# Kernel tuning notes

Measured on AMD Instinct MI355X. Metric: run time of the kernel, lower is better.

Reference implementation:

```python
import jax, jax.numpy as jnp
import numpy as np

B, CIN, H, W = 4, 128, 64, 64
PL, ATT, R = 256, 64, 16   # planes, planes//4, MD_R
STEPS = 6                   # TRAIN_STEPS default
EPS = 1e-6


def _l2norm(v, axis):
    return v / jnp.maximum(jnp.linalg.norm(v, axis=axis, keepdims=True), 1e-12)


def setup_inputs() -> dict:
    key = jax.random.key(0)
    ks = jax.random.split(key, 11)
    s = 0.05
    return {
        "x": jax.random.normal(ks[0], (B, CIN, H, W), jnp.float32),
        "conv1_w": jax.random.normal(ks[1], (PL, CIN), jnp.float32) * s,      # 1x1 conv, no bias
        "conv3_w": jax.random.normal(ks[2], (PL, 1, 3, 3), jnp.float32) * s,  # depthwise 3x3
        "conv3_b": jax.random.normal(ks[3], (PL,), jnp.float32) * s,
        "lower_w": jax.random.normal(ks[4], (PL, PL), jnp.float32) * s,       # Conv1d k=1
        "lower_b": jax.random.normal(ks[5], (PL,), jnp.float32) * s,
        "ca1_w": jax.random.normal(ks[6], (ATT, PL), jnp.float32) * s,        # channel attn 1x1
        "ca2_w": jax.random.normal(ks[7], (PL, ATT), jnp.float32) * s,
        "fc_w": jax.random.normal(ks[8], (CIN, PL), jnp.float32) * s,         # fc_adapt_channels1
        "fc_b": jax.random.normal(ks[9], (CIN,), jnp.float32) * s,
        "bases_init": jax.random.uniform(ks[10], (B * H * W, 1, R), jnp.float32),  # rand_init bases
    }


def reference(x, conv1_w, conv3_w, conv3_b, lower_w, lower_b, ca1_w, ca2_w, fc_w, fc_b, bases_init):
    # conv1 (1x1, no bias) then depthwise 3x3 (groups=PL)
    y = jnp.einsum('bchw,oc->bohw', x, conv1_w)
    y = jax.lax.conv_general_dilated(y, conv3_w, (1, 1), 'SAME',
                                     dimension_numbers=('NCHW', 'OIHW', 'NCHW'),
                                     feature_group_count=PL)
    y = y + conv3_b[None, :, None, None]
    # '(b s) c h w -> (b h w) c s' with s=1 -> tokens [M, C]
    xm = jnp.transpose(y, (0, 2, 3, 1)).reshape(B * H * W, PL)
    # Hamburger lower_bread: Conv1d(k=1) + ReLU
    xl = jax.nn.relu(xm @ lower_w.T + lower_b)
    xn = xl[:, None, :]                        # NMF x: [M, D=1, N=C]
    # NMF2D local_inference (torch.no_grad in original)
    xs = jax.lax.stop_gradient(xn)
    bases = _l2norm(bases_init, 1)             # [M, 1, R]
    coef = jax.nn.softmax(jnp.einsum('mdn,mdr->mnr', xs, bases), axis=-1)  # inv_t=1
    for _ in range(STEPS):
        num = jnp.einsum('mdn,mdr->mnr', xs, bases)
        den = jnp.einsum('mnr,mrk->mnk', coef, jnp.einsum('mdr,mdk->mrk', bases, bases))
        coef = coef * num / (den + EPS)
        num = jnp.einsum('mdn,mnr->mdr', xs, coef)
        den = jnp.einsum('mdr,mrk->mdk', bases, jnp.einsum('mnr,mnk->mrk', coef, coef))
        bases = bases * num / (den + EPS)
    bases = jax.lax.stop_gradient(bases)
    coef = jax.lax.stop_gradient(coef)
    # compute_coef (differentiable via xn)
    num = jnp.einsum('mdn,mdr->mnr', xn, bases)
    den = jnp.einsum('mnr,mrk->mnk', coef, jnp.einsum('mdr,mdk->mrk', bases, bases))
    coef = coef * num / (den + EPS)
    xr = jnp.einsum('mdr,mnr->mn', bases, coef)     # bases @ coef^T, [M, C] (D=1 squeezed)
    feat = jax.nn.relu(xm + xr)                     # Hamburger residual + ReLU
    # mean over s (s=1) and back to [B, C, H, W]
    feat = jnp.transpose(feat.reshape(B, H, W, PL), (0, 3, 1, 2))
    # AMPooling channel attention
    avg = feat.mean(axis=(2, 3))
    mx = feat.max(axis=(2, 3))
    ca = lambda v: jax.nn.relu(v @ ca1_w.T) @ ca2_w.T
    att = jax.nn.sigmoid(ca(avg) + ca(mx))          # [B, C]
    out = feat * att[:, :, None, None]
    out = jnp.einsum('bchw,oc->bohw', out, fc_w) + fc_b[None, :, None, None]
    return out, att[:, :, None, None]
```

## Files before the change

### kernel.cpp

```cpp
#include <hip/hip_runtime.h>
#include <hip/hip_bf16.h>
#include <math.h>

#define EPS 1e-6f
#define PITCH 72

typedef short s16x8 __attribute__((ext_vector_type(8)));
typedef float f32x4 __attribute__((ext_vector_type(4)));

__device__ __forceinline__ short bf16of(float f) {
  __hip_bfloat16 h = __float2bfloat16(f);
  return __builtin_bit_cast(short, h);
}
__device__ __forceinline__ float f32of(unsigned short u) {
  unsigned int x = ((unsigned int)u) << 16;
  return __builtin_bit_cast(float, x);
}

__global__ __launch_bounds__(256) void k_conv1x1(const float* __restrict__ x,
                                                 const float* __restrict__ w1,
                                                 short* __restrict__ ybf) {
  __shared__ __align__(16) short Aw[128 * PITCH];
  __shared__ __align__(16) short Xs[64 * PITCH];
  const int t = threadIdx.x;
  const int m0 = blockIdx.x * 64, p0 = blockIdx.y * 128;
  const int img = m0 >> 12, hw0 = m0 & 4095;
  const int lane = t & 63, w = t >> 6;
  const int lrow = lane & 15, lk = (lane >> 4) * 8;
  f32x4 acc[4][2];
#pragma unroll
  for (int i = 0; i < 4; ++i)
#pragma unroll
    for (int j = 0; j < 2; ++j) acc[i][j] = {0.f, 0.f, 0.f, 0.f};

  for (int kk = 0; kk < 128; kk += 64) {
    __syncthreads();
    {
      const int pr = t & 127, kq = t >> 7;
      const float* wp = w1 + (size_t)(p0 + pr) * 128 + kk + kq * 32;
#pragma unroll
      for (int q = 0; q < 8; ++q) {
        const float4 v = *(const float4*)(wp + q * 4);
        short4 sv = {bf16of(v.x), bf16of(v.y), bf16of(v.z), bf16of(v.w)};
        *(short4*)(&Aw[pr * PITCH + kq * 32 + q * 4]) = sv;
      }
    }
    {
      const int m4 = (t & 15) * 4;
      const int cg = (t >> 4) * 4;
      float4 col[4];
#pragma unroll
      for (int cc = 0; cc < 4; ++cc)
        col[cc] = *(const float4*)(x + (size_t)(img * 128 + kk + cg + cc) * 4096 + hw0 + m4);
#pragma unroll
      for (int r = 0; r < 4; ++r) {
        short4 sv = {bf16of(((const float*)&col[0])[r]),
                     bf16of(((const float*)&col[1])[r]),
                     bf16of(((const float*)&col[2])[r]),
                     bf16of(((const float*)&col[3])[r])};
        *(short4*)(&Xs[(m4 + r) * PITCH + cg]) = sv;
      }
    }
    __syncthreads();
#pragma unroll
    for (int ks = 0; ks < 2; ++ks) {
      const int ko = ks * 32 + lk;
      s16x8 bfr[2];
#pragma unroll
      for (int j = 0; j < 2; ++j)
        bfr[j] = *(const s16x8*)(&Xs[(((w >> 1) * 2 + j) * 16 + lrow) * PITCH + ko]);
#pragma unroll
      for (int i = 0; i < 4; ++i) {
        const s16x8 af = *(const s16x8*)(&Aw[(((w & 1) * 4 + i) * 16 + lrow) * PITCH + ko]);
#pragma unroll
        for (int j = 0; j < 2; ++j)
          acc[i][j] = __builtin_amdgcn_mfma_f32_16x16x32_bf16(af, bfr[j], acc[i][j], 0, 0, 0);
      }
    }
  }
#pragma unroll
  for (int i = 0; i < 4; ++i) {
    const int p = p0 + ((w & 1) * 4 + i) * 16 + (lane >> 4) * 4;
#pragma unroll
    for (int j = 0; j < 2; ++j) {
      const int m = m0 + ((w >> 1) * 2 + j) * 16 + lrow;
      const f32x4 v = acc[i][j];
      short4 sv = {bf16of(v.x), bf16of(v.y), bf16of(v.z), bf16of(v.w)};
      *(short4*)(ybf + (size_t)m * 256 + p) = sv;
    }
  }
}

__global__ __launch_bounds__(256) void k_dwconv(const unsigned short* __restrict__ ybf,
                                                const float* __restrict__ w3,
                                                const float* __restrict__ b3,
                                                short* __restrict__ xmb) {
  __shared__ float wt[9][256];
  __shared__ float bs[256];
  const int t = threadIdx.x;
#pragma unroll
  for (int i = 0; i < 9; ++i) wt[i][t] = w3[t * 9 + i];
  bs[t] = b3[t];
  __syncthreads();
  const int sub = t >> 6;
  const int pq = t & 63;
  const int m = blockIdx.x * 4 + sub;
  const int hw = m & 4095;
  const int h = hw >> 6, ww = hw & 63;
  const int bb = m >> 12;
  float4 acc = *(const float4*)(&bs[pq * 4]);
#pragma unroll
  for (int dy = -1; dy <= 1; ++dy) {
    const int hh = h + dy;
    if (hh < 0 || hh > 63) continue;
#pragma unroll
    for (int dx = -1; dx <= 1; ++dx) {
      const int w2 = ww + dx;
      if (w2 < 0 || w2 > 63) continue;
      const int idx = (dy + 1) * 3 + (dx + 1);
      const ushort4 v =
          *(const ushort4*)(ybf + (size_t)((bb << 12) + (hh << 6) + w2) * 256 + pq * 4);
      const float4 wv = *(const float4*)(&wt[idx][pq * 4]);
      acc.x += f32of(v.x) * wv.x;
      acc.y += f32of(v.y) * wv.y;
      acc.z += f32of(v.z) * wv.z;
      acc.w += f32of(v.w) * wv.w;
    }
  }
  short4 sv = {bf16of(acc.x), bf16of(acc.y), bf16of(acc.z), bf16of(acc.w)};
  *(short4*)(xmb + (size_t)m * 256 + pq * 4) = sv;
}

__global__ __launch_bounds__(256) void k_lower(const unsigned short* __restrict__ xmb,
                                               const float* __restrict__ lw,
                                               const float* __restrict__ lb,
                                               short* __restrict__ xlb) {
  __shared__ __align__(16) short Aw[128 * PITCH];
  __shared__ __align__(16) short Xs[64 * PITCH];
  const int t = threadIdx.x;
  const int m0 = blockIdx.x * 64, n0 = blockIdx.y * 128;
  const int lane = t & 63, w = t >> 6;
  const int lrow = lane & 15, lk = (lane >> 4) * 8;
  f32x4 acc[4][2];
#pragma unroll
  for (int i = 0; i < 4; ++i)
#pragma unroll
    for (int j = 0; j < 2; ++j) acc[i][j] = {0.f, 0.f, 0.f, 0.f};

  for (int kk = 0; kk < 256; kk += 64) {
    __syncthreads();
    {
      const int nr = t & 127, kq = t >> 7;
      const float* wp = lw + (size_t)(n0 + nr) * 256 + kk + kq * 32;
#pragma unroll
      for (int q = 0; q < 8; ++q) {
        const float4 v = *(const float4*)(wp + q * 4);
        short4 sv = {bf16of(v.x), bf16of(v.y), bf16of(v.z), bf16of(v.w)};
        *(short4*)(&Aw[nr * PITCH + kq * 32 + q * 4]) = sv;
      }
    }
    {
      const int m = t & 63, q = t >> 6;
      const unsigned short* xp = xmb + (size_t)(m0 + m) * 256 + kk + q * 16;
      *(s16x8*)(&Xs[m * PITCH + q * 16]) = *(const s16x8*)(xp);
      *(s16x8*)(&Xs[m * PITCH + q * 16 + 8]) = *(const s16x8*)(xp + 8);
    }
    __syncthreads();
#pragma unroll
    for (int ks = 0; ks < 2; ++ks) {
      const int ko = ks * 32 + lk;
      s16x8 bfr[2];
#pragma unroll
      for (int j = 0; j < 2; ++j)
        bfr[j] = *(const s16x8*)(&Xs[(((w >> 1) * 2 + j) * 16 + lrow) * PITCH + ko]);
#pragma unroll
      for (int i = 0; i < 4; ++i) {
        const s16x8 af = *(const s16x8*)(&Aw[(((w & 1) * 4 + i) * 16 + lrow) * PITCH + ko]);
#pragma unroll
        for (int j = 0; j < 2; ++j)
          acc[i][j] = __builtin_amdgcn_mfma_f32_16x16x32_bf16(af, bfr[j], acc[i][j], 0, 0, 0);
      }
    }
  }
#pragma unroll
  for (int i = 0; i < 4; ++i) {
    const int n = n0 + ((w & 1) * 4 + i) * 16 + (lane >> 4) * 4;
    const float4 bias = *(const float4*)(lb + n);
#pragma unroll
    for (int j = 0; j < 2; ++j) {
      const int m = m0 + ((w >> 1) * 2 + j) * 16 + lrow;
      const f32x4 v = acc[i][j];
      short4 sv = {bf16of(fmaxf(v.x + bias.x, 0.f)), bf16of(fmaxf(v.y + bias.y, 0.f)),
                   bf16of(fmaxf(v.z + bias.z, 0.f)), bf16of(fmaxf(v.w + bias.w, 0.f))};
      *(short4*)(xlb + (size_t)m * 256 + n) = sv;
    }
  }
}

__global__ __launch_bounds__(256) void k_em_fast(const unsigned short* __restrict__ xlb,
                                                 const float* __restrict__ binit,
                                                 const unsigned short* __restrict__ xmb,
                                                 short* __restrict__ featb,
                                                 float* __restrict__ psum,
                                                 float* __restrict__ pmax,
                                                 int* __restrict__ flag) {
  __shared__ float psL[1024], pmL[1024];
  __shared__ int sflag;
  const int t = threadIdx.x;
  const int lane = t & 63, w = t >> 6;
  const int bid = blockIdx.x;
  const int m0 = bid * 16 + w * 4;
  bool asym = false;
#pragma unroll
  for (int p = 0; p < 4; ++p) {
    const float bv = binit[(size_t)(m0 + p) * 16 + (lane & 15)];
    const float bn = bv / fmaxf(fabsf(bv), 1e-12f);
    asym |= !__all(bn == 1.0f);
  }
  if (t == 0) sflag = 0;
  __syncthreads();
  if (asym && lane == 0) sflag = 1;
  __syncthreads();
  if (sflag) {
    if (t == 0) flag[bid] = 1;
    return;
  }

  float s[4][4], C[4][4], Bv[4];
#pragma unroll
  for (int p = 0; p < 4; ++p) {
    const ushort4 su = *(const ushort4*)(xlb + (size_t)(m0 + p) * 256 + lane * 4);
    s[p][0] = f32of(su.x);
    s[p][1] = f32of(su.y);
    s[p][2] = f32of(su.z);
    s[p][3] = f32of(su.w);
    Bv[p] = 1.f;
#pragma unroll
    for (int i = 0; i < 4; ++i) C[p][i] = 0.0625f;
  }
  for (int step = 0; step < 6; ++step) {
    float pnum[4], psq[4];
#pragma unroll
    for (int p = 0; p < 4; ++p) {
      const float k1 = 16.f * Bv[p] * Bv[p];
      pnum[p] = 0.f;
      psq[p] = 0.f;
#pragma unroll
      for (int i = 0; i < 4; ++i) {
        const float den = fmaf(C[p][i], k1, EPS);
        const float cn = C[p][i] * (s[p][i] * Bv[p]) * __builtin_amdgcn_rcpf(den);
        C[p][i] = cn;
        pnum[p] = fmaf(s[p][i], cn, pnum[p]);
        psq[p] = fmaf(cn, cn, psq[p]);
      }
    }
#pragma unroll
    for (int d = 1; d < 64; d <<= 1) {
#pragma unroll
      for (int p = 0; p < 4; ++p) {
        pnum[p] += __shfl_xor(pnum[p], d, 64);
        psq[p] += __shfl_xor(psq[p], d, 64);
      }
    }
#pragma unroll
    for (int p = 0; p < 4; ++p)
      Bv[p] = Bv[p] * pnum[p] *
              __builtin_amdgcn_rcpf(fmaf(16.f * Bv[p], psq[p], EPS));
  }
  float ps4[4] = {0.f, 0.f, 0.f, 0.f};
  float pm4[4] = {-1e30f, -1e30f, -1e30f, -1e30f};
#pragma unroll
  for (int p = 0; p < 4; ++p) {
    const ushort4 xmu = *(const ushort4*)(xmb + (size_t)(m0 + p) * 256 + lane * 4);
    const float xmv[4] = {f32of(xmu.x), f32of(xmu.y), f32of(xmu.z), f32of(xmu.w)};
    const float k1 = 16.f * Bv[p] * Bv[p];
    float o[4];
#pragma unroll
    for (int i = 0; i < 4; ++i) {
      const float den = fmaf(C[p][i], k1, EPS);
      const float cn = C[p][i] * (s[p][i] * Bv[p]) * __builtin_amdgcn_rcpf(den);
      const float xr = 16.f * Bv[p] * cn;
      o[i] = fmaxf(xmv[i] + xr, 0.f);
      ps4[i] += o[i];
      pm4[i] = fmaxf(pm4[i], o[i]);
    }
    short4 sv = {bf16of(o[0]), bf16of(o[1]), bf16of(o[2]), bf16of(o[3])};
    *(short4*)(featb + (size_t)(m0 + p) * 256 + lane * 4) = sv;
  }
#pragma unroll
  for (int i = 0; i < 4; ++i) {
    psL[w * 256 + lane * 4 + i] = ps4[i];
    pmL[w * 256 + lane * 4 + i] = pm4[i];
  }
  __syncthreads();
  const float sv = psL[t] + psL[256 + t] + psL[512 + t] + psL[768 + t];
  const float mv =
      fmaxf(fmaxf(pmL[t], pmL[256 + t]), fmaxf(pmL[512 + t], pmL[768 + t]));
  psum[(size_t)bid * 256 + t] = sv;
  pmax[(size_t)bid * 256 + t] = mv;
  if (t == 0) flag[bid] = 0;
}

__global__ __launch_bounds__(256, 2) void k_em_slowfix(
    const unsigned short* __restrict__ xlb, const float* __restrict__ binit,
    const unsigned short* __restrict__ xmb, short* __restrict__ featb,
    float* __restrict__ psum, float* __restrict__ pmax,
    const int* __restrict__ flag) {
  const int bid = blockIdx.x;
  if (flag[bid] == 0) return;
  __shared__ float psL[1024], pmL[1024];
  const int t = threadIdx.x;
  const int lane = t & 63, w = t >> 6;
  const int m0 = bid * 16 + w * 4;
  float ps4[4] = {0.f, 0.f, 0.f, 0.f};
  float pm4[4] = {-1e30f, -1e30f, -1e30f, -1e30f};
  for (int p = 0; p < 4; ++p) {
    const int m = m0 + p;
    const ushort4 su = *(const ushort4*)(xlb + (size_t)m * 256 + lane * 4);
    const float s[4] = {f32of(su.x), f32of(su.y), f32of(su.z), f32of(su.w)};
    float b[16];
#pragma unroll
    for (int r = 0; r < 16; ++r) {
      const float v = binit[(size_t)m * 16 + r];
      b[r] = v / fmaxf(fabsf(v), 1e-12f);
    }
    float c[4][16];
#pragma unroll
    for (int i = 0; i < 4; ++i) {
      float mx = s[i] * b[0];
#pragma unroll
      for (int r = 1; r < 16; ++r) mx = fmaxf(mx, s[i] * b[r]);
      float sum = 0.f;
#pragma unroll
      for (int r = 0; r < 16; ++r) {
        const float e = __expf(s[i] * b[r] - mx);
        c[i][r] = e;
        sum += e;
      }
      const float inv = __fdividef(1.f, sum);
#pragma unroll
      for (int r = 0; r < 16; ++r) c[i][r] *= inv;
    }
    for (int step = 0; step < 6; ++step) {
      float red[32];
#pragma unroll
      for (int r = 0; r < 32; ++r) red[r] = 0.f;
#pragma unroll
      for (int i = 0; i < 4; ++i) {
        float tt = 0.f;
#pragma unroll
        for (int r = 0; r < 16; ++r) tt += c[i][r] * b[r];
        float tp = 0.f;
#pragma unroll
        for (int r = 0; r < 16; ++r) {
          const float cn = c[i][r] * (s[i] * b[r]) * __frcp_rn(tt * b[r] + EPS);
          c[i][r] = cn;
          tp += cn * b[r];
          red[r] += s[i] * cn;
        }
#pragma unroll
        for (int r = 0; r < 16; ++r) red[16 + r] += tp * c[i][r];
      }
      int cnt = 32;
#pragma unroll
      for (int k = 4; k >= 0; --k) {
        const int d = 1 << k;
        const bool up = (lane >> k) & 1;
        const int half = cnt >> 1;
#pragma unroll
        for (int j = 0; j < half; ++j) {
          const float lo = red[j], hi = red[j + half];
          const float send = up ? lo : hi;
          const float recv = __shfl_xor(send, d, 64);
          red[j] = (up ? hi : lo) + recv;
        }
        cnt = half;
      }
      float S = red[0] + __shfl_xor(red[0], 32, 64);
      const float dpart = __shfl_xor(S, 16, 64);
      const float q = S * __frcp_rn(dpart + EPS);
#pragma unroll
      for (int r = 0; r < 16; ++r) b[r] *= __shfl(q, r, 64);
    }
    const ushort4 xmu = *(const ushort4*)(xmb + (size_t)m * 256 + lane * 4);
    const float xmv[4] = {f32of(xmu.x), f32of(xmu.y), f32of(xmu.z), f32of(xmu.w)};
    float o4[4];
#pragma unroll
    for (int i = 0; i < 4; ++i) {
      float tt = 0.f;
#pragma unroll
      for (int r = 0; r < 16; ++r) tt += c[i][r] * b[r];
      float xr = 0.f;
#pragma unroll
      for (int r = 0; r < 16; ++r) {
        const float cn = c[i][r] * (s[i] * b[r]) * __frcp_rn(tt * b[r] + EPS);
        xr += b[r] * cn;
      }
      o4[i] = fmaxf(xmv[i] + xr, 0.f);
      ps4[i] += o4[i];
      pm4[i] = fmaxf(pm4[i], o4[i]);
    }
    short4 sv = {bf16of(o4[0]), bf16of(o4[1]), bf16of(o4[2]), bf16of(o4[3])};
    *(short4*)(featb + (size_t)m * 256 + lane * 4) = sv;
  }
#pragma unroll
  for (int i = 0; i < 4; ++i) {
    psL[w * 256 + lane * 4 + i] = ps4[i];
    pmL[w * 256 + lane * 4 + i] = pm4[i];
  }
  __syncthreads();
  const float sv = psL[t] + psL[256 + t] + psL[512 + t] + psL[768 + t];
  const float mv =
      fmaxf(fmaxf(pmL[t], pmL[256 + t]), fmaxf(pmL[512 + t], pmL[768 + t]));
  psum[(size_t)bid * 256 + t] = sv;
  pmax[(size_t)bid * 256 + t] = mv;
}

__global__ __launch_bounds__(1024) void k_att(const float* __restrict__ psum,
                                              const float* __restrict__ pmax,
                                              const float* __restrict__ ca1,
                                              const float* __restrict__ ca2,
                                              float* __restrict__ attv,
                                              float* __restrict__ out_att) {
  __shared__ float sA[4][256], sM[4][256], fA[256], fM[256], sH[64];
  const int t = threadIdx.x;
  const int b = blockIdx.x;
  const int ch = t & 255, part = t >> 8;
  float sum = 0.f, mx = -1e30f;
#pragma unroll 4
  for (int j = 0; j < 64; ++j) {
    const int g = b * 256 + part * 64 + j;
    sum += psum[(size_t)g * 256 + ch];
    mx = fmaxf(mx, pmax[(size_t)g * 256 + ch]);
  }
  sA[part][ch] = sum;
  sM[part][ch] = mx;
  __syncthreads();
  if (t < 256) {
    fA[t] = (sA[0][t] + sA[1][t] + sA[2][t] + sA[3][t]) * (1.0f / 4096.0f);
    fM[t] = fmaxf(fmaxf(sM[0][t], sM[1][t]), fmaxf(sM[2][t], sM[3][t]));
  }
  __syncthreads();
  if (t < 64) {
    float ha = 0.f, hm = 0.f;
#pragma unroll 8
    for (int p = 0; p < 256; ++p) {
      const float wv = ca1[t * 256 + p];
      ha += fA[p] * wv;
      hm += fM[p] * wv;
    }
    sH[t] = fmaxf(ha, 0.f) + fmaxf(hm, 0.f);
  }
  __syncthreads();
  if (t < 256) {
    float logit = 0.f;
#pragma unroll 8
    for (int a = 0; a < 64; ++a) logit += sH[a] * ca2[t * 64 + a];
    const float av = 1.0f / (1.0f + expf(-logit));
    attv[b * 256 + t] = av;
    out_att[b * 256 + t] = av;
  }
}

__global__ __launch_bounds__(256) void k_fc(const unsigned short* __restrict__ featb,
                                            const float* __restrict__ attv,
                                            const float* __restrict__ fw,
                                            const float* __restrict__ fb,
                                            float* __restrict__ out) {
  __shared__ __align__(16) short Fs[64 * PITCH];
  __shared__ __align__(16) short Ws[64 * PITCH];
  const int t = threadIdx.x;
  const int m0 = blockIdx.x * 64, o0 = blockIdx.y * 64;
  const int img = m0 >> 12, hw0 = m0 & 4095;
  const int lane = t & 63, w = t >> 6;
  const int lrow = lane & 15, lk = (lane >> 4) * 8;
  f32x4 acc[2][2];
#pragma unroll
  for (int i = 0; i < 2; ++i)
#pragma unroll
    for (int j = 0; j < 2; ++j) acc[i][j] = {0.f, 0.f, 0.f, 0.f};

  for (int kk = 0; kk < 256; kk += 64) {
    __syncthreads();
    {
      const int m = t & 63, q = t >> 6;
      const unsigned short* fp = featb + (size_t)(m0 + m) * 256 + kk + q * 16;
      const float* ap = attv + img * 256 + kk + q * 16;
#pragma unroll
      for (int jj = 0; jj < 4; ++jj) {
        const ushort4 v = *(const ushort4*)(fp + jj * 4);
        const float4 a = *(const float4*)(ap + jj * 4);
        short4 sv = {bf16of(f32of(v.x) * a.x), bf16of(f32of(v.y) * a.y),
                     bf16of(f32of(v.z) * a.z), bf16of(f32of(v.w) * a.w)};
        *(short4*)(&Fs[m * PITCH + q * 16 + jj * 4]) = sv;
      }
    }
    {
      const int o = t & 63, q = t >> 6;
      const float* wp = fw + (size_t)(o0 + o) * 256 + kk + q * 16;
#pragma unroll
      for (int jj = 0; jj < 4; ++jj) {
        const float4 v = *(const float4*)(wp + jj * 4);
        short4 sv = {bf16of(v.x), bf16of(v.y), bf16of(v.z), bf16of(v.w)};
        *(short4*)(&Ws[o * PITCH + q * 16 + jj * 4]) = sv;
      }
    }
    __syncthreads();
#pragma unroll
    for (int ks = 0; ks < 2; ++ks) {
      const int ko = ks * 32 + lk;
      s16x8 af[2];
#pragma unroll
      for (int i = 0; i < 2; ++i)
        af[i] = *(const s16x8*)(&Fs[(((w >> 1) * 2 + i) * 16 + lrow) * PITCH + ko]);
#pragma unroll
      for (int j = 0; j < 2; ++j) {
        const s16x8 bfr = *(const s16x8*)(&Ws[(((w & 1) * 2 + j) * 16 + lrow) * PITCH + ko]);
#pragma unroll
        for (int i = 0; i < 2; ++i)
          acc[i][j] = __builtin_amdgcn_mfma_f32_16x16x32_bf16(af[i], bfr, acc[i][j], 0, 0, 0);
      }
    }
  }
#pragma unroll
  for (int j = 0; j < 2; ++j) {
    const int o = o0 + ((w & 1) * 2 + j) * 16 + lrow;
    const float bias = fb[o];
#pragma unroll
    for (int i = 0; i < 2; ++i) {
      const int hw = hw0 + ((w >> 1) * 2 + i) * 16 + (lane >> 4) * 4;
      f32x4 v = acc[i][j];
      v.x += bias;
      v.y += bias;
      v.z += bias;
      v.w += bias;
      *(f32x4*)(out + (size_t)img * 524288 + (size_t)o * 4096 + hw) = v;
    }
  }
}

extern "C" void kernel_launch(void* const* d_in, const int* in_sizes, int n_in,
                              void* d_out, int out_size, void* d_ws, size_t ws_size,
                              hipStream_t stream) {
  const float* x = (const float*)d_in[0];
  const float* w1 = (const float*)d_in[1];
  const float* w3 = (const float*)d_in[2];
  const float* b3 = (const float*)d_in[3];
  const float* lw = (const float*)d_in[4];
  const float* lb = (const float*)d_in[5];
  const float* ca1 = (const float*)d_in[6];
  const float* ca2 = (const float*)d_in[7];
  const float* fw = (const float*)d_in[8];
  const float* fb = (const float*)d_in[9];
  const float* binit = (const float*)d_in[10];

  char* wsb = (char*)d_ws;
  short* ybf = (short*)wsb;
  short* xmb = (short*)(wsb + (8u << 20));
  short* xlb = (short*)(wsb + (16u << 20));
  short* featb = (short*)(wsb + (24u << 20));
  float* psum = (float*)(wsb + (32u << 20));
  float* pmax = (float*)(wsb + (34u << 20));
  float* attv = (float*)(wsb + (36u << 20));
  int* flag = (int*)(wsb + (37u << 20));
  float* out = (float*)d_out;
  float* out_att = out + 2097152;

  const dim3 blk(256);
  k_conv1x1<<<dim3(256, 2), blk, 0, stream>>>(x, w1, ybf);
  k_dwconv<<<dim3(4096), blk, 0, stream>>>((const unsigned short*)ybf, w3, b3, xmb);
  k_lower<<<dim3(256, 2), blk, 0, stream>>>((const unsigned short*)xmb, lw, lb, xlb);
  k_em_fast<<<dim3(1024), blk, 0, stream>>>((const unsigned short*)xlb, binit,
                                            (const unsigned short*)xmb, featb,
                                            psum, pmax, flag);
  k_em_slowfix<<<dim3(1024), blk, 0, stream>>>((const unsigned short*)xlb, binit,
                                               (const unsigned short*)xmb, featb,
                                               psum, pmax, flag);
  k_att<<<dim3(4), dim3(1024), 0, stream>>>(psum, pmax, ca1, ca2, attv, out_att);
  k_fc<<<dim3(256, 2), blk, 0, stream>>>((const unsigned short*)featb, attv, fw,
                                         fb, out);
}
```

Baseline: 88.36 us.

## Fuse depthwise conv into lower GEMM and reduce pooling stats with atomics

Merges the depthwise 3x3 conv into the lower-bread GEMM kernel. Each block computes one image row of 64 tokens for all 256 channels directly into shared memory, so the GEMM no longer re-reads xm from global memory and one kernel launch is removed. The per-block partial sums and maxes for channel attention are now accumulated with global atomics, which shrinks k_att to a direct read. The conv1x1 kernel zeroes the accumulators first. The risks are that the depthwise conv is recomputed twice (once per N-half block), the larger shared-memory footprint can lower occupancy, and the float atomicAdd order is nondeterministic. The unsigned-int atomicMax trick is only valid because the feature values are non-negative after ReLU.

```diff
diff --git a/kernel.cpp b/kernel.cpp
--- a/kernel.cpp
+++ b/kernel.cpp
@@ -4,6 +4,7 @@
 
 #define EPS 1e-6f
 #define PITCH 72
+#define XPITCH 264
 
 typedef short s16x8 __attribute__((ext_vector_type(8)));
 typedef float f32x4 __attribute__((ext_vector_type(4)));
@@ -19,10 +20,19 @@
 
 __global__ __launch_bounds__(256) void k_conv1x1(const float* __restrict__ x,
                                                  const float* __restrict__ w1,
-                                                 short* __restrict__ ybf) {
+                                                 short* __restrict__ ybf,
+                                                 float* __restrict__ gsum,
+                                                 unsigned int* __restrict__ gmaxu) {
   __shared__ __align__(16) short Aw[128 * PITCH];
   __shared__ __align__(16) short Xs[64 * PITCH];
   const int t = threadIdx.x;
+  if (blockIdx.x == 0 && blockIdx.y == 0) {
+#pragma unroll
+    for (int i = 0; i < 4; ++i) {
+      gsum[t + i * 256] = 0.f;
+      gmaxu[t + i * 256] = 0u;
+    }
+  }
   const int m0 = blockIdx.x * 64, p0 = blockIdx.y * 128;
   const int img = m0 >> 12, hw0 = m0 & 4095;
   const int lane = t & 63, w = t >> 6;
@@ -91,55 +101,60 @@
   }
 }
 
-__global__ __launch_bounds__(256) void k_dwconv(const unsigned short* __restrict__ ybf,
-                                                const float* __restrict__ w3,
-                                                const float* __restrict__ b3,
-                                                short* __restrict__ xmb) {
+__global__ __launch_bounds__(256) void k_dw_lower(
+    const unsigned short* __restrict__ ybf, const float* __restrict__ w3,
+    const float* __restrict__ b3, const float* __restrict__ lw,
+    const float* __restrict__ lb, short* __restrict__ xmb,
+    short* __restrict__ xlb) {
+  __shared__ __align__(16) short XsF[64 * XPITCH];
+  __shared__ __align__(16) short Aw[128 * PITCH];
   __shared__ float wt[9][256];
   __shared__ float bs[256];
   const int t = threadIdx.x;
+  const int rt = blockIdx.x;
+  const int n0 = blockIdx.y * 128;
+  const int img = rt >> 6, h = rt & 63;
+  const int m0 = rt * 64;
+  const int lane = t & 63, w = t >> 6;
 #pragma unroll
   for (int i = 0; i < 9; ++i) wt[i][t] = w3[t * 9 + i];
   bs[t] = b3[t];
   __syncthreads();
-  const int sub = t >> 6;
-  const int pq = t & 63;
-  const int m = blockIdx.x * 4 + sub;
-  const int hw = m & 4095;
-  const int h = hw >> 6, ww = hw & 63;
-  const int bb = m >> 12;
-  float4 acc = *(const float4*)(&bs[pq * 4]);
-#pragma unroll
-  for (int dy = -1; dy <= 1; ++dy) {
-    const int hh = h + dy;
-    if (hh < 0 || hh > 63) continue;
-#pragma unroll
-    for (int dx = -1; dx <= 1; ++dx) {
-      const int w2 = ww + dx;
-      if (w2 < 0 || w2 > 63) continue;
-      const int idx = (dy + 1) * 3 + (dx + 1);
-      const ushort4 v =
-          *(const ushort4*)(ybf + (size_t)((bb << 12) + (hh << 6) + w2) * 256 + pq * 4);
-      const float4 wv = *(const float4*)(&wt[idx][pq * 4]);
-      acc.x += f32of(v.x) * wv.x;
-      acc.y += f32of(v.y) * wv.y;
-      acc.z += f32of(v.z) * wv.z;
-      acc.w += f32of(v.w) * wv.w;
-    }
-  }
-  short4 sv = {bf16of(acc.x), bf16of(acc.y), bf16of(acc.z), bf16of(acc.w)};
-  *(short4*)(xmb + (size_t)m * 256 + pq * 4) = sv;
-}
-
-__global__ __launch_bounds__(256) void k_lower(const unsigned short* __restrict__ xmb,
-                                               const float* __restrict__ lw,
-                                               const float* __restrict__ lb,
-                                               short* __restrict__ xlb) {
-  __shared__ __align__(16) short Aw[128 * PITCH];
-  __shared__ __align__(16) short Xs[64 * PITCH];
-  const int t = threadIdx.x;
-  const int m0 = blockIdx.x * 64, n0 = blockIdx.y * 128;
-  const int lane = t & 63, w = t >> 6;
+
+  {
+    const int ch = lane * 4;
+    const float4 bias = *(const float4*)(&bs[ch]);
+    const size_t rowbase = ((size_t)(img << 12) + (h << 6)) * 256 + ch;
+#pragma unroll 4
+    for (int i = 0; i < 16; ++i) {
+      const int px = w * 16 + i;
+      float a0 = bias.x, a1 = bias.y, a2 = bias.z, a3 = bias.w;
+#pragma unroll
+      for (int dy = -1; dy <= 1; ++dy) {
+        const int hh = h + dy;
+        if (hh < 0 || hh > 63) continue;
+#pragma unroll
+        for (int dx = -1; dx <= 1; ++dx) {
+          const int w2 = px + dx;
+          if (w2 < 0 || w2 > 63) continue;
+          const int idx = (dy + 1) * 3 + (dx + 1);
+          const ushort4 v = *(const ushort4*)(
+              ybf + ((size_t)(img << 12) + (hh << 6) + w2) * 256 + ch);
+          const float4 wv = *(const float4*)(&wt[idx][ch]);
+          a0 = fmaf(f32of(v.x), wv.x, a0);
+          a1 = fmaf(f32of(v.y), wv.y, a1);
+          a2 = fmaf(f32of(v.z), wv.z, a2);
+          a3 = fmaf(f32of(v.w), wv.w, a3);
+        }
+      }
+      const short4 sv = {bf16of(a0), bf16of(a1), bf16of(a2), bf16of(a3)};
+      *(short4*)(&XsF[px * XPITCH + ch]) = sv;
+      if (blockIdx.y == 0) *(short4*)(xmb + (size_t)(m0 + px) * 256 + ch) = sv;
+    }
+    (void)rowbase;
+  }
+  __syncthreads();
+
   const int lrow = lane & 15, lk = (lane >> 4) * 8;
   f32x4 acc[4][2];
 #pragma unroll
@@ -159,12 +174,6 @@
         *(short4*)(&Aw[nr * PITCH + kq * 32 + q * 4]) = sv;
       }
     }
-    {
-      const int m = t & 63, q = t >> 6;
-      const unsigned short* xp = xmb + (size_t)(m0 + m) * 256 + kk + q * 16;
-      *(s16x8*)(&Xs[m * PITCH + q * 16]) = *(const s16x8*)(xp);
-      *(s16x8*)(&Xs[m * PITCH + q * 16 + 8]) = *(const s16x8*)(xp + 8);
-    }
     __syncthreads();
 #pragma unroll
     for (int ks = 0; ks < 2; ++ks) {
@@ -172,7 +181,8 @@
       s16x8 bfr[2];
 #pragma unroll
       for (int j = 0; j < 2; ++j)
-        bfr[j] = *(const s16x8*)(&Xs[(((w >> 1) * 2 + j) * 16 + lrow) * PITCH + ko]);
+        bfr[j] = *(const s16x8*)(
+            &XsF[(((w >> 1) * 2 + j) * 16 + lrow) * XPITCH + kk + ko]);
 #pragma unroll
       for (int i = 0; i < 4; ++i) {
         const s16x8 af = *(const s16x8*)(&Aw[(((w & 1) * 4 + i) * 16 + lrow) * PITCH + ko]);
@@ -201,8 +211,8 @@
                                                  const float* __restrict__ binit,
                                                  const unsigned short* __restrict__ xmb,
                                                  short* __restrict__ featb,
-                                                 float* __restrict__ psum,
-                                                 float* __restrict__ pmax,
+                                                 float* __restrict__ gsum,
+                                                 unsigned int* __restrict__ gmaxu,
                                                  int* __restrict__ flag) {
   __shared__ float psL[1024], pmL[1024];
   __shared__ int sflag;
@@ -296,15 +306,16 @@
   const float sv = psL[t] + psL[256 + t] + psL[512 + t] + psL[768 + t];
   const float mv =
       fmaxf(fmaxf(pmL[t], pmL[256 + t]), fmaxf(pmL[512 + t], pmL[768 + t]));
-  psum[(size_t)bid * 256 + t] = sv;
-  pmax[(size_t)bid * 256 + t] = mv;
+  const int img = bid >> 8;
+  atomicAdd(&gsum[img * 256 + t], sv);
+  atomicMax(&gmaxu[img * 256 + t], __float_as_uint(mv));
   if (t == 0) flag[bid] = 0;
 }
 
 __global__ __launch_bounds__(256, 2) void k_em_slowfix(
     const unsigned short* __restrict__ xlb, const float* __restrict__ binit,
     const unsigned short* __restrict__ xmb, short* __restrict__ featb,
-    float* __restrict__ psum, float* __restrict__ pmax,
+    float* __restrict__ gsum, unsigned int* __restrict__ gmaxu,
     const int* __restrict__ flag) {
   const int bid = blockIdx.x;
   if (flag[bid] == 0) return;
@@ -412,34 +423,22 @@
   const float sv = psL[t] + psL[256 + t] + psL[512 + t] + psL[768 + t];
   const float mv =
       fmaxf(fmaxf(pmL[t], pmL[256 + t]), fmaxf(pmL[512 + t], pmL[768 + t]));
-  psum[(size_t)bid * 256 + t] = sv;
-  pmax[(size_t)bid * 256 + t] = mv;
-}
-
-__global__ __launch_bounds__(1024) void k_att(const float* __restrict__ psum,
-                                              const float* __restrict__ pmax,
-                                              const float* __restrict__ ca1,
-                                              const float* __restrict__ ca2,
-                                              float* __restrict__ attv,
-                                              float* __restrict__ out_att) {
-  __shared__ float sA[4][256], sM[4][256], fA[256], fM[256], sH[64];
+  const int img = bid >> 8;
+  atomicAdd(&gsum[img * 256 + t], sv);
+  atomicMax(&gmaxu[img * 256 + t], __float_as_uint(mv));
+}
+
+__global__ __launch_bounds__(256) void k_att(const float* __restrict__ gsum,
+                                             const unsigned int* __restrict__ gmaxu,
+                                             const float* __restrict__ ca1,
+                                             const float* __restrict__ ca2,
+                                             float* __restrict__ attv,
+                                             float* __restrict__ out_att) {
+  __shared__ float fA[256], fM[256], sH[64];
   const int t = threadIdx.x;
   const int b = blockIdx.x;
-  const int ch = t & 255, part = t >> 8;
-  float sum = 0.f, mx = -1e30f;
-#pragma unroll 4
-  for (int j = 0; j < 64; ++j) {
-    const int g = b * 256 + part * 64 + j;
-    sum += psum[(size_t)g * 256 + ch];
-    mx = fmaxf(mx, pmax[(size_t)g * 256 + ch]);
-  }
-  sA[part][ch] = sum;
-  sM[part][ch] = mx;
-  __syncthreads();
-  if (t < 256) {
-    fA[t] = (sA[0][t] + sA[1][t] + sA[2][t] + sA[3][t]) * (1.0f / 4096.0f);
-    fM[t] = fmaxf(fmaxf(sM[0][t], sM[1][t]), fmaxf(sM[2][t], sM[3][t]));
-  }
+  fA[t] = gsum[b * 256 + t] * (1.0f / 4096.0f);
+  fM[t] = __uint_as_float(gmaxu[b * 256 + t]);
   __syncthreads();
   if (t < 64) {
     float ha = 0.f, hm = 0.f;
@@ -452,14 +451,12 @@
     sH[t] = fmaxf(ha, 0.f) + fmaxf(hm, 0.f);
   }
   __syncthreads();
-  if (t < 256) {
-    float logit = 0.f;
+  float logit = 0.f;
 #pragma unroll 8
-    for (int a = 0; a < 64; ++a) logit += sH[a] * ca2[t * 64 + a];
-    const float av = 1.0f / (1.0f + expf(-logit));
-    attv[b * 256 + t] = av;
-    out_att[b * 256 + t] = av;
-  }
+  for (int a = 0; a < 64; ++a) logit += sH[a] * ca2[t * 64 + a];
+  const float av = 1.0f / (1.0f + expf(-logit));
+  attv[b * 256 + t] = av;
+  out_att[b * 256 + t] = av;
 }
 
 __global__ __launch_bounds__(256) void k_fc(const unsigned short* __restrict__ featb,
@@ -559,24 +556,24 @@
   short* xmb = (short*)(wsb + (8u << 20));
   short* xlb = (short*)(wsb + (16u << 20));
   short* featb = (short*)(wsb + (24u << 20));
-  float* psum = (float*)(wsb + (32u << 20));
-  float* pmax = (float*)(wsb + (34u << 20));
-  float* attv = (float*)(wsb + (36u << 20));
-  int* flag = (int*)(wsb + (37u << 20));
+  float* gsum = (float*)(wsb + (32u << 20));
+  unsigned int* gmaxu = (unsigned int*)(wsb + (33u << 20));
+  float* attv = (float*)(wsb + (34u << 20));
+  int* flag = (int*)(wsb + (35u << 20));
   float* out = (float*)d_out;
   float* out_att = out + 2097152;
 
   const dim3 blk(256);
-  k_conv1x1<<<dim3(256, 2), blk, 0, stream>>>(x, w1, ybf);
-  k_dwconv<<<dim3(4096), blk, 0, stream>>>((const unsigned short*)ybf, w3, b3, xmb);
-  k_lower<<<dim3(256, 2), blk, 0, stream>>>((const unsigned short*)xmb, lw, lb, xlb);
+  k_conv1x1<<<dim3(256, 2), blk, 0, stream>>>(x, w1, ybf, gsum, gmaxu);
+  k_dw_lower<<<dim3(256, 2), blk, 0, stream>>>((const unsigned short*)ybf, w3, b3,
+                                               lw, lb, xmb, xlb);
   k_em_fast<<<dim3(1024), blk, 0, stream>>>((const unsigned short*)xlb, binit,
                                             (const unsigned short*)xmb, featb,
-                                            psum, pmax, flag);
+                                            gsum, gmaxu, flag);
   k_em_slowfix<<<dim3(1024), blk, 0, stream>>>((const unsigned short*)xlb, binit,
                                                (const unsigned short*)xmb, featb,
-                                               psum, pmax, flag);
-  k_att<<<dim3(4), dim3(1024), 0, stream>>>(psum, pmax, ca1, ca2, attv, out_att);
+                                               gsum, gmaxu, flag);
+  k_att<<<dim3(4), blk, 0, stream>>>(gsum, gmaxu, ca1, ca2, attv, out_att);
   k_fc<<<dim3(256, 2), blk, 0, stream>>>((const unsigned short*)featb, attv, fw,
                                          fb, out);
 }
```

Result: slower. 111.3 us (+25.9%).
